# Kernel tuning notes

Hardware: AMD Instinct MI355X
Metric: run time of the kernel (lower is better)

The kernel has to match this reference:

```python
import jax, jax.numpy as jnp
import numpy as np

N, D = 8192, 128
NOISEVAR = 1.0

def _softplusinverse(v):
    return np.log(1.0 - np.exp(-v)) + v

def setup_inputs() -> dict:
    key = jax.random.key(0)
    kx, kn = jax.random.split(key)
    x = jax.random.normal(kx, (N, D), dtype=jnp.float32)
    noise = jax.random.normal(kn, (N, D), dtype=jnp.float32)
    phi = jnp.asarray(_softplusinverse(NOISEVAR), dtype=jnp.float32)
    return {"x": x, "phi": phi, "noise": noise}

def reference(x, phi, noise):
    # x: [n, d] encoded features; phi: scalar noise param; noise: [n, d] i.i.d. N(0,1)
    n = x.shape[0]
    var = jax.nn.softplus(phi)
    # Pairwise squared L2 distances via Gram-matrix trick (same math as
    # norm(x_i - x_j)^2, avoids the [n, n, d] broadcast intermediate).
    sq = jnp.sum(x * x, axis=1)                                  # [n]
    d2 = jnp.maximum(sq[:, None] + sq[None, :] - 2.0 * (x @ x.T), 0.0)  # [n, n]
    kde_contribution = jnp.mean(jax.nn.logsumexp(-0.5 * d2 / var, axis=1))
    IXT_nats = jnp.log(jnp.float32(n)) - kde_contribution
    IXT = IXT_nats / jnp.log(jnp.float32(2.0))  # bits=True -> nats2bits
    out = x + var * noise                        # training=True noise injection
    return out, IXT
```

## Files before the change

### kernel.cpp

```cpp
#include <hip/hip_runtime.h>
#include <hip/hip_bf16.h>

#define N 8192
#define D 128
#define TILE 128
#define JCHUNK 8

typedef __attribute__((ext_vector_type(8))) short short8;
typedef __attribute__((ext_vector_type(4))) float floatx4;
typedef unsigned int u32;

#define GLOAD_LDS16(g, l) \
    __builtin_amdgcn_global_load_lds((const __attribute__((address_space(1))) u32*)(g), \
                                     (__attribute__((address_space(3))) u32*)(l), 16, 0, 0)

static __device__ inline float softplus_of(const float* __restrict__ phi) {
    float p = phi[0];
    return (p > 20.f) ? p : log1pf(__expf(p));
}

static __device__ inline unsigned short f2bf(float f) {
    return __builtin_bit_cast(unsigned short, __float2bfloat16(f));
}

static __device__ inline short8 pack8(float4 a, float4 b) {
    short8 r;
    r[0] = (short)f2bf(a.x); r[1] = (short)f2bf(a.y);
    r[2] = (short)f2bf(a.z); r[3] = (short)f2bf(a.w);
    r[4] = (short)f2bf(b.x); r[5] = (short)f2bf(b.y);
    r[6] = (short)f2bf(b.z); r[7] = (short)f2bf(b.w);
    return r;
}

__global__ __launch_bounds__(256) void k1_cvt(
        const float* __restrict__ x, unsigned short* __restrict__ bf16x,
        float* __restrict__ sq, float* __restrict__ rowsum) {
    int gid = blockIdx.x * 256 + threadIdx.x;
    int row = gid >> 4;
    int gc  = gid & 15;
    const float* src = x + (size_t)row * D + gc * 8;
    float4 u = *(const float4*)src;
    float4 v = *(const float4*)(src + 4);
    short8 p = pack8(u, v);
    int gp = gc ^ (row & 15);
    *(short8*)&bf16x[(size_t)row * D + gp * 8] = p;

    float s = 0.f;
    #pragma unroll
    for (int k = 0; k < 8; k++) {
        u32 bits = ((u32)(unsigned short)p[k]) << 16;
        float b = __builtin_bit_cast(float, bits);
        s += b * b;
    }
    #pragma unroll
    for (int m = 1; m < 16; m <<= 1) s += __shfl_xor(s, m, 64);
    if (gc == 0) { sq[row] = s; rowsum[row] = 0.f; }
}

__global__ __launch_bounds__(256, 2) void k2_gram(
        const unsigned short* __restrict__ bf16x, const float* __restrict__ phi,
        const float* __restrict__ sq, float* __restrict__ rowsum) {
    __shared__ __align__(16) unsigned short Bs[2][TILE * D];

    const int t = threadIdx.x;
    const int wave = t >> 6;
    const int lane = t & 63;
    const int lrow = lane & 15;
    const int quad = lane >> 4;
    const int wr = (wave & 1) * 64;
    const int wc = (wave >> 1) * 64;
    const int iBase  = blockIdx.x * TILE;
    const int jBase0 = blockIdx.y * (JCHUNK * TILE);

    float var = softplus_of(phi);
    float ninvvar = -0.5f / var;

    short8 af[4][4];
    #pragma unroll
    for (int mt = 0; mt < 4; mt++) {
        const unsigned short* arow = bf16x + (size_t)(iBase + wr + mt * 16 + lrow) * D;
        #pragma unroll
        for (int kk = 0; kk < 4; kk++)
            af[mt][kk] = *(const short8*)&arow[((kk * 4 + quad) ^ lrow) * 8];
    }
    float si[4][4];
    #pragma unroll
    for (int mt = 0; mt < 4; mt++)
        #pragma unroll
        for (int reg = 0; reg < 4; reg++)
            si[mt][reg] = sq[iBase + wr + mt * 16 + quad * 4 + reg];

    float rowAcc[4][4] = {};

    {
        const unsigned short* src = bf16x + (size_t)jBase0 * D;
        #pragma unroll
        for (int s = 0; s < 8; s++) {
            int cb = s * 256 + wave * 64;
            GLOAD_LDS16(src + (size_t)(cb + lane) * 8, &Bs[0][cb * 8]);
        }
    }
    __syncthreads();

    for (int jt = 0; jt < JCHUNK; ++jt) {
        if (jt + 1 < JCHUNK) {
            const unsigned short* src = bf16x + (size_t)(jBase0 + (jt + 1) * TILE) * D;
            unsigned short* dstb = Bs[(jt + 1) & 1];
            #pragma unroll
            for (int s = 0; s < 8; s++) {
                int cb = s * 256 + wave * 64;
                GLOAD_LDS16(src + (size_t)(cb + lane) * 8, &dstb[cb * 8]);
            }
        }

        const unsigned short* B = Bs[jt & 1];
        floatx4 acc[4][4] = {};
        #pragma unroll
        for (int kk = 0; kk < 4; kk++) {
            short8 bfr[4];
            #pragma unroll
            for (int nt = 0; nt < 4; nt++) {
                int R = wc + nt * 16 + lrow;
                bfr[nt] = *(const short8*)&B[(size_t)R * D + (((kk * 4 + quad) ^ lrow) * 8)];
            }
            #pragma unroll
            for (int mt = 0; mt < 4; mt++)
                #pragma unroll
                for (int nt = 0; nt < 4; nt++)
                    acc[mt][nt] = __builtin_amdgcn_mfma_f32_16x16x32_bf16(
                        af[mt][kk], bfr[nt], acc[mt][nt], 0, 0, 0);
        }

        const int jBase = jBase0 + jt * TILE;
        float sqj[4];
        #pragma unroll
        for (int nt = 0; nt < 4; nt++)
            sqj[nt] = sq[jBase + wc + nt * 16 + lrow];
        #pragma unroll
        for (int mt = 0; mt < 4; mt++) {
            #pragma unroll
            for (int reg = 0; reg < 4; reg++) {
                float s0 = si[mt][reg];
                #pragma unroll
                for (int nt = 0; nt < 4; nt++) {
                    float g  = acc[mt][nt][reg];
                    float d2 = fmaxf(fmaf(-2.f, g, s0 + sqj[nt]), 0.f);
                    rowAcc[mt][reg] += __expf(d2 * ninvvar);
                }
            }
        }

        __syncthreads();
    }

    #pragma unroll
    for (int mt = 0; mt < 4; mt++) {
        #pragma unroll
        for (int reg = 0; reg < 4; reg++) {
            float v = rowAcc[mt][reg];
            #pragma unroll
            for (int m = 1; m < 16; m <<= 1) v += __shfl_xor(v, m, 64);
            if (lrow == 0)
                atomicAdd(&rowsum[iBase + wr + mt * 16 + quad * 4 + reg], v);
        }
    }
}

__global__ __launch_bounds__(1024) void k3_final(
        const float* __restrict__ rowsum, float* __restrict__ out_ixt) {
    __shared__ float red[16];
    int t = threadIdx.x;
    float local = 0.f;
    for (int i = t; i < N; i += 1024) local += logf(rowsum[i]);
    #pragma unroll
    for (int m = 1; m < 64; m <<= 1) local += __shfl_xor(local, m, 64);
    if ((t & 63) == 0) red[t >> 6] = local;
    __syncthreads();
    if (t < 16) {
        float v = red[t];
        #pragma unroll
        for (int m = 1; m < 16; m <<= 1) v += __shfl_xor(v, m, 64);
        if (t == 0) {
            float kde = v / (float)N;
            out_ixt[0] = (logf((float)N) - kde) * 1.4426950408889634f;
        }
    }
}

__global__ __launch_bounds__(256) void k4_noise(
        const float4* __restrict__ x, const float* __restrict__ phi,
        const float4* __restrict__ noise, float4* __restrict__ out) {
    int i = blockIdx.x * 256 + threadIdx.x;
    float var = softplus_of(phi);
    float4 xv = x[i], nv = noise[i];
    float4 ov;
    ov.x = xv.x + var * nv.x;
    ov.y = xv.y + var * nv.y;
    ov.z = xv.z + var * nv.z;
    ov.w = xv.w + var * nv.w;
    out[i] = ov;
}

extern "C" void kernel_launch(void* const* d_in, const int* in_sizes, int n_in,
                              void* d_out, int out_size, void* d_ws, size_t ws_size,
                              hipStream_t stream) {
    const float* x     = (const float*)d_in[0];
    const float* phi   = (const float*)d_in[1];
    const float* noise = (const float*)d_in[2];
    float* out = (float*)d_out;

    float* rowsum = (float*)d_ws;
    float* sq     = rowsum + N;
    unsigned short* bf16x = (unsigned short*)d_out;

    k1_cvt<<<(N * 16) / 256, 256, 0, stream>>>(x, bf16x, sq, rowsum);
    dim3 g2(N / TILE, N / (TILE * JCHUNK));
    k2_gram<<<g2, 256, 0, stream>>>(bf16x, phi, sq, rowsum);
    k3_final<<<1, 1024, 0, stream>>>(rowsum, out + (size_t)N * D);
    k4_noise<<<(N * D / 4) / 256, 256, 0, stream>>>(
        (const float4*)x, phi, (const float4*)noise, (float4*)out);
}
```

Measured before the change: 101.4 us.

## Exploit Gram symmetry: compute upper-triangle tiles only with row and column sums

Makes the Gram/KDE kernel visit only upper-triangular 128x128 tile pairs (2080 tiles over 512 blocks of 4-5 tiles each). Each off-diagonal tile adds its exp values both to its row sums and, via column reductions and atomics, to the transposed rows, roughly halving MFMA and exp work. The exponent is also folded into an exp2 with the scale premultiplied into the squared norms. It adds A-fragment reloads when the row tile changes, more atomics, and slightly uneven load across blocks.

After: 97.11 us. 4.3% less time.

```diff
diff --git a/kernel.cpp b/kernel.cpp
--- a/kernel.cpp
+++ b/kernel.cpp
@@ -4,7 +4,7 @@
 #define N 8192
 #define D 128
 #define TILE 128
-#define JCHUNK 8
+#define NT (N / TILE)
 
 typedef __attribute__((ext_vector_type(8))) short short8;
 typedef __attribute__((ext_vector_type(4))) float floatx4;
@@ -69,31 +69,21 @@
     const int quad = lane >> 4;
     const int wr = (wave & 1) * 64;
     const int wc = (wave >> 1) * 64;
-    const int iBase  = blockIdx.x * TILE;
-    const int jBase0 = blockIdx.y * (JCHUNK * TILE);
+
+    const int b = blockIdx.x;
+    const int cnt   = (b < 32) ? 5 : 4;
+    const int start = (b < 32) ? 5 * b : 160 + 4 * (b - 32);
+
+    int pti = 0, rem = start, len = NT;
+    while (rem >= len) { rem -= len; ++pti; --len; }
+    int ptj = pti + rem;
 
     float var = softplus_of(phi);
-    float ninvvar = -0.5f / var;
-
-    short8 af[4][4];
-    #pragma unroll
-    for (int mt = 0; mt < 4; mt++) {
-        const unsigned short* arow = bf16x + (size_t)(iBase + wr + mt * 16 + lrow) * D;
-        #pragma unroll
-        for (int kk = 0; kk < 4; kk++)
-            af[mt][kk] = *(const short8*)&arow[((kk * 4 + quad) ^ lrow) * 8];
-    }
-    float si[4][4];
-    #pragma unroll
-    for (int mt = 0; mt < 4; mt++)
-        #pragma unroll
-        for (int reg = 0; reg < 4; reg++)
-            si[mt][reg] = sq[iBase + wr + mt * 16 + quad * 4 + reg];
-
-    float rowAcc[4][4] = {};
+    const float e2c = (-0.5f / var) * 1.4426950408889634f;
+    const float m2c = -2.0f * e2c;
 
     {
-        const unsigned short* src = bf16x + (size_t)jBase0 * D;
+        const unsigned short* src = bf16x + (size_t)ptj * TILE * D;
         #pragma unroll
         for (int s = 0; s < 8; s++) {
             int cb = s * 256 + wave * 64;
@@ -102,10 +92,38 @@
     }
     __syncthreads();
 
-    for (int jt = 0; jt < JCHUNK; ++jt) {
-        if (jt + 1 < JCHUNK) {
-            const unsigned short* src = bf16x + (size_t)(jBase0 + (jt + 1) * TILE) * D;
-            unsigned short* dstb = Bs[(jt + 1) & 1];
+    short8 af[4][4];
+    float sie[4][4];
+    float rowAcc[4][4];
+    int curTi = -1;
+
+    auto flushRow = [&]() {
+        const int iBase = curTi * TILE;
+        #pragma unroll
+        for (int mt = 0; mt < 4; mt++)
+            #pragma unroll
+            for (int reg = 0; reg < 4; reg++) {
+                float v = rowAcc[mt][reg];
+                #pragma unroll
+                for (int m = 1; m < 16; m <<= 1) v += __shfl_xor(v, m, 64);
+                if (lrow == 0)
+                    atomicAdd(&rowsum[iBase + wr + mt * 16 + quad * 4 + reg], v);
+            }
+    };
+
+    for (int r = 0; r < cnt; ++r) {
+        const int jBase = ptj * TILE;
+
+        float sje[4];
+        #pragma unroll
+        for (int nt = 0; nt < 4; nt++)
+            sje[nt] = sq[jBase + wc + nt * 16 + lrow] * e2c;
+
+        int nti = pti, ntj = ptj + 1;
+        if (ntj == NT) { ++nti; ntj = nti; }
+        if (r + 1 < cnt) {
+            const unsigned short* src = bf16x + (size_t)ntj * TILE * D;
+            unsigned short* dstb = Bs[(r + 1) & 1];
             #pragma unroll
             for (int s = 0; s < 8; s++) {
                 int cb = s * 256 + wave * 64;
@@ -113,7 +131,28 @@
             }
         }
 
-        const unsigned short* B = Bs[jt & 1];
+        if (pti != curTi) {
+            if (curTi >= 0) flushRow();
+            const int iBase = pti * TILE;
+            #pragma unroll
+            for (int mt = 0; mt < 4; mt++) {
+                const unsigned short* arow =
+                    bf16x + (size_t)(iBase + wr + mt * 16 + lrow) * D;
+                #pragma unroll
+                for (int kk = 0; kk < 4; kk++)
+                    af[mt][kk] = *(const short8*)&arow[((kk * 4 + quad) ^ lrow) * 8];
+            }
+            #pragma unroll
+            for (int mt = 0; mt < 4; mt++)
+                #pragma unroll
+                for (int reg = 0; reg < 4; reg++) {
+                    sie[mt][reg] = sq[iBase + wr + mt * 16 + quad * 4 + reg] * e2c;
+                    rowAcc[mt][reg] = 0.f;
+                }
+            curTi = pti;
+        }
+
+        const unsigned short* B = Bs[r & 1];
         floatx4 acc[4][4] = {};
         #pragma unroll
         for (int kk = 0; kk < 4; kk++) {
@@ -121,7 +160,7 @@
             #pragma unroll
             for (int nt = 0; nt < 4; nt++) {
                 int R = wc + nt * 16 + lrow;
-                bfr[nt] = *(const short8*)&B[(size_t)R * D + (((kk * 4 + quad) ^ lrow) * 8)];
+                bfr[nt] = *(const short8*)&B[(size_t)R * D + ((kk * 4 + quad) ^ lrow) * 8];
             }
             #pragma unroll
             for (int mt = 0; mt < 4; mt++)
@@ -131,39 +170,38 @@
                         af[mt][kk], bfr[nt], acc[mt][nt], 0, 0, 0);
         }
 
-        const int jBase = jBase0 + jt * TILE;
-        float sqj[4];
-        #pragma unroll
-        for (int nt = 0; nt < 4; nt++)
-            sqj[nt] = sq[jBase + wc + nt * 16 + lrow];
+        float colAcc[4] = {0.f, 0.f, 0.f, 0.f};
         #pragma unroll
         for (int mt = 0; mt < 4; mt++) {
             #pragma unroll
             for (int reg = 0; reg < 4; reg++) {
-                float s0 = si[mt][reg];
+                float base = sie[mt][reg];
                 #pragma unroll
                 for (int nt = 0; nt < 4; nt++) {
-                    float g  = acc[mt][nt][reg];
-                    float d2 = fmaxf(fmaf(-2.f, g, s0 + sqj[nt]), 0.f);
-                    rowAcc[mt][reg] += __expf(d2 * ninvvar);
+                    float p2 = fminf(fmaf(acc[mt][nt][reg], m2c, base + sje[nt]), 0.f);
+                    float p = exp2f(p2);
+                    rowAcc[mt][reg] += p;
+                    colAcc[nt] += p;
                 }
             }
         }
 
+        if (pti != ptj) {
+            #pragma unroll
+            for (int nt = 0; nt < 4; nt++) {
+                float v = colAcc[nt];
+                v += __shfl_xor(v, 16, 64);
+                v += __shfl_xor(v, 32, 64);
+                if (quad == 0)
+                    atomicAdd(&rowsum[jBase + wc + nt * 16 + lrow], v);
+            }
+        }
+
+        pti = nti; ptj = ntj;
         __syncthreads();
     }
 
-    #pragma unroll
-    for (int mt = 0; mt < 4; mt++) {
-        #pragma unroll
-        for (int reg = 0; reg < 4; reg++) {
-            float v = rowAcc[mt][reg];
-            #pragma unroll
-            for (int m = 1; m < 16; m <<= 1) v += __shfl_xor(v, m, 64);
-            if (lrow == 0)
-                atomicAdd(&rowsum[iBase + wr + mt * 16 + quad * 4 + reg], v);
-        }
-    }
+    flushRow();
 }
 
 __global__ __launch_bounds__(1024) void k3_final(
@@ -214,8 +252,7 @@
     unsigned short* bf16x = (unsigned short*)d_out;
 
     k1_cvt<<<(N * 16) / 256, 256, 0, stream>>>(x, bf16x, sq, rowsum);
-    dim3 g2(N / TILE, N / (TILE * JCHUNK));
-    k2_gram<<<g2, 256, 0, stream>>>(bf16x, phi, sq, rowsum);
+    k2_gram<<<512, 256, 0, stream>>>(bf16x, phi, sq, rowsum);
     k3_final<<<1, 1024, 0, stream>>>(rowsum, out + (size_t)N * D);
     k4_noise<<<(N * D / 4) / 256, 256, 0, stream>>>(
         (const float4*)x, phi, (const float4*)noise, (float4*)out);
```
